# Optimization experiments

Measured on AMD Instinct MI355X. Metric: run time of the kernel, lower is better.

Reference implementation:

```python
import jax, jax.numpy as jnp
import numpy as np

# FUME epipolar image translation: for each output pixel p2=(x2,y2) the fundamental
# matrix F maps it to a line l = F @ [x2*d, y2*d, 1] in the input view (full-res
# coordinates; d = per-batch downsampling factor). The output value is the line
# integral of the input image along that epipolar line, computed by stepping one
# pixel at a time along the dominant axis with bilinear (1-D linear) interpolation
# across the other axis; out-of-bounds samples contribute zero.

def _translate(img, F, d):
    B, C, H, W = img.shape
    dt = img.dtype
    yy, xx = jnp.meshgrid(jnp.arange(H, dtype=dt), jnp.arange(W, dtype=dt), indexing='ij')
    db = d[:, None, None].astype(dt)                          # (B,1,1)
    px, py = xx[None] * db, yy[None] * db                     # (B,H,W) full-res coords
    a = F[0, 0] * px + F[0, 1] * py + F[0, 2]                 # line coeffs l = F @ [x,y,1]
    b = F[1, 0] * px + F[1, 1] * py + F[1, 2]
    c = F[2, 0] * px + F[2, 1] * py + F[2, 2]
    horiz = jnp.abs(b) >= jnp.abs(a)                          # dominant axis per pixel

    db4 = db[..., None]                                       # (B,1,1,1)
    # horizontal traversal: step over columns s, solve a*(s*d) + b*(y*d) + c = 0
    s = jnp.arange(W, dtype=dt)
    denom_h = jnp.where(horiz, b, jnp.ones((), dt))[..., None] * db4
    yline = -(a[..., None] * (s * db4) + c[..., None]) / denom_h    # (B,H,W,W)
    # vertical traversal: step over rows t, solve for x
    t = jnp.arange(H, dtype=dt)
    denom_v = jnp.where(horiz, jnp.ones((), dt), a)[..., None] * db4
    xline = -(b[..., None] * (t * db4) + c[..., None]) / denom_v    # (B,H,W,H)

    def sample_one(imgb, y, x):
        # imgb: (C,H,W); y: (H,W,W) row coord per column step; x: (H,W,H) col coord per row step
        y0 = jnp.floor(y)
        wy = y - y0
        y0i = jnp.clip(y0.astype(jnp.int32), 0, H - 1)
        y1i = jnp.clip(y0i + 1, 0, H - 1)
        cols = jnp.arange(W)
        vh = (1 - wy)[None] * imgb[:, y0i, cols] + wy[None] * imgb[:, y1i, cols]  # (C,H,W,W)
        vh = jnp.where(((y >= 0) & (y <= H - 1))[None], vh, jnp.zeros((), imgb.dtype)).sum(-1)

        x0 = jnp.floor(x)
        wx = x - x0
        x0i = jnp.clip(x0.astype(jnp.int32), 0, W - 1)
        x1i = jnp.clip(x0i + 1, 0, W - 1)
        rows = jnp.arange(H)
        vv = (1 - wx)[None] * imgb[:, rows, x0i] + wx[None] * imgb[:, rows, x1i]  # (C,H,W,H)
        vv = jnp.where(((x >= 0) & (x <= W - 1))[None], vv, jnp.zeros((), imgb.dtype)).sum(-1)
        return vh, vv

    vh, vv = jax.vmap(sample_one)(img, yline, xline)          # each (B,C,H,W)
    return jnp.where(horiz[:, None], vh, vv)


def setup_inputs() -> dict:
    key = jax.random.key(0)
    k1, k2, k3 = jax.random.split(key, 3)
    B, C, H, W = 4, 4, 128, 128
    view1 = jax.random.normal(k1, (B, C, H, W), jnp.float32)
    F21 = jax.random.normal(k2, (3, 3), jnp.float32)
    F12 = jax.random.normal(k3, (3, 3), jnp.float32)
    downsampled_factor = jnp.ones((B,), jnp.float32)
    return {"view1": view1, "F21": F21, "F12": F12, "downsampled_factor": downsampled_factor}


def reference(view1, F21, F12, downsampled_factor):
    # forward uses F21 only; F12 is kept for the backward pass in the original module
    return _translate(view1, F21, downsampled_factor)
```

## Files before the change

kernel.cpp:

```cpp
#include <hip/hip_runtime.h>


#define CC 4
#define HH 128
#define WW 128

__global__ void fume_stage(const float* __restrict__ img, float* __restrict__ ws) {
    __shared__ float tile[4][32][33];
    int tx0 = blockIdx.x * 32, ty0 = blockIdx.y * 32, b = blockIdx.z;
    int tx = threadIdx.x, ty = threadIdx.y;
    const float* src = img + (size_t)b * CC * HH * WW;
    #pragma unroll
    for (int ch = 0; ch < 4; ++ch)
        #pragma unroll
        for (int i = ty; i < 32; i += 8)
            tile[ch][i][tx] = src[(ch * HH + ty0 + i) * WW + tx0 + tx];
    __syncthreads();
    float4* base_h = (float4*)ws + (size_t)b * 32768;
    float4* base_v = base_h + 16384;
    #pragma unroll
    for (int i = ty; i < 32; i += 8) {
        float4 v = make_float4(tile[0][i][tx], tile[1][i][tx],
                               tile[2][i][tx], tile[3][i][tx]);
        base_v[(ty0 + i) * WW + (tx0 + tx)] = v;
        float4 h = make_float4(tile[0][tx][i], tile[1][tx][i],
                               tile[2][tx][i], tile[3][tx][i]);
        base_h[(tx0 + i) * HH + (ty0 + tx)] = h;
    }
}

__global__ void __launch_bounds__(512) fume_kernel(
        const float4* __restrict__ cubes,
        const float* __restrict__ F,
        const float* __restrict__ dsf,
        float* __restrict__ out) {
    int tx  = threadIdx.x;
    int seg = threadIdx.y;
    int x = blockIdx.x * 64 + tx;
    int y = blockIdx.y;
    int b = blockIdx.z;

    float d = dsf[b];
    float F00 = F[0], F01 = F[1], F02 = F[2];
    float F10 = F[3], F11 = F[4], F12 = F[5];
    float F20 = F[6], F21 = F[7], F22 = F[8];

    float px = __fmul_rn((float)x, d);
    float py = __fmul_rn((float)y, d);
    float av = __fadd_rn(__fadd_rn(__fmul_rn(F00, px), __fmul_rn(F01, py)), F02);
    float bv = __fadd_rn(__fadd_rn(__fmul_rn(F10, px), __fmul_rn(F11, py)), F12);
    float cv = __fadd_rn(__fadd_rn(__fmul_rn(F20, px), __fmul_rn(F21, py)), F22);

    bool horiz  = fabsf(bv) >= fabsf(av);
    float ncoef = horiz ? av : bv;
    float den   = __fmul_rn(horiz ? bv : av, d);
    float nrec  = -__fdiv_rn(1.0f, den);

    const float4* P = cubes + (size_t)b * 32768 + (horiz ? 0 : 16384);

    float A  = __fmul_rn(__fmul_rn(ncoef, d), nrec);
    float Bc = __fmul_rn(cv, nrec);
    int lkmin, lkmax;
    if (fabsf(A) > 1e-20f) {
        float inv = 1.0f / A;
        float k1 = (0.0f   - Bc) * inv;
        float k2 = (127.0f - Bc) * inv;
        float lo = fminf(k1, k2) - 2.0f;
        float hi = fmaxf(k1, k2) + 2.0f;
        lo = fmaxf(lo, 0.0f);
        hi = fminf(hi, 127.0f);
        if (lo > hi || !(lo == lo)) { lkmin = 1; lkmax = 0; }
        else { lkmin = (int)lo; lkmax = (int)hi; }
    } else {
        bool full = (Bc >= 0.0f) && (Bc <= 127.0f);
        lkmin = full ? 0 : 1;
        lkmax = full ? 127 : 0;
    }
    int wkmin = lkmin, wkmax = lkmax;
    #pragma unroll
    for (int off = 1; off < 64; off <<= 1) {
        wkmin = min(wkmin, __shfl_xor(wkmin, off));
        wkmax = max(wkmax, __shfl_xor(wkmax, off));
    }

    float a0 = 0.f, a1 = 0.f, a2 = 0.f, a3 = 0.f;
    int len = wkmax - wkmin + 1;
    if (len > 0) {
        int cnt = (len + 7) >> 3;
        int ks  = wkmin + seg * cnt;
        int ke  = min(ks + cnt - 1, wkmax);
        #pragma unroll 4
        for (int k = ks; k <= ke; ++k) {
            float m  = __fmul_rn((float)k, d);
            float q  = __fadd_rn(__fmul_rn(ncoef, m), cv);
            float u  = __fmul_rn(q, nrec);
            bool ok  = (u >= 0.f) && (u <= 127.f);
            int i0   = (int)floorf(u);
            i0 = max(0, min(i0, 126));
            float w  = __fsub_rn(u, (float)i0);
            float wz  = ok ? w : 0.f;
            float omw = ok ? __fsub_rn(1.f, w) : 0.f;
            const float4* row = P + k * 128;
            float4 q0 = row[i0];
            float4 q1 = row[i0 + 1];
            a0 = fmaf(omw, q0.x, a0); a0 = fmaf(wz, q1.x, a0);
            a1 = fmaf(omw, q0.y, a1); a1 = fmaf(wz, q1.y, a1);
            a2 = fmaf(omw, q0.z, a2); a2 = fmaf(wz, q1.z, a2);
            a3 = fmaf(omw, q0.w, a3); a3 = fmaf(wz, q1.w, a3);
        }
    }

    __shared__ float part[8][4][64];
    part[seg][0][tx] = a0;
    part[seg][1][tx] = a1;
    part[seg][2][tx] = a2;
    part[seg][3][tx] = a3;
    __syncthreads();

    if (seg < 4) {
        int ch = seg;
        float s = part[0][ch][tx];
        #pragma unroll
        for (int t = 1; t < 8; ++t) s = __fadd_rn(s, part[t][ch][tx]);
        out[(((size_t)b * CC + ch) * HH + y) * WW + x] = s;
    }
}

extern "C" void kernel_launch(void* const* d_in, const int* in_sizes, int n_in,
                              void* d_out, int out_size, void* d_ws, size_t ws_size,
                              hipStream_t stream) {
    const float* view1 = (const float*)d_in[0];
    const float* F21   = (const float*)d_in[1];
    const float* dsf   = (const float*)d_in[3];

    const int B = in_sizes[3];

    dim3 stb(32, 8, 1);
    dim3 stg(WW / 32, HH / 32, B);
    fume_stage<<<stg, stb, 0, stream>>>(view1, (float*)d_ws);

    dim3 ftb(64, 8, 1);
    dim3 ftg(WW / 64, HH, B);
    fume_kernel<<<ftg, ftb, 0, stream>>>((const float4*)d_ws, F21, dsf,
                                         (float*)d_out);
}
```

Before: 70.41 us.

## Pack neighbor pairs as fp16 and use fdot2 for interpolation

The staging kernel now stores each texel together with its right (or lower) neighbor as packed fp16 pairs for four channels in one 16-byte entry. The main loop then issues one gather per step instead of two and does the 2-tap interpolation with fdot2 instructions. This halves gather traffic and instruction count in the hot loop. The cost is fp16 precision on both image values and weights, which may exceed the reference tolerance. The staging tile also grows by one row and column to hold the halo.

```diff
diff --git a/kernel.cpp b/kernel.cpp
--- a/kernel.cpp
+++ b/kernel.cpp
@@ -5,27 +5,50 @@
 #define HH 128
 #define WW 128
 
-__global__ void fume_stage(const float* __restrict__ img, float* __restrict__ ws) {
-    __shared__ float tile[4][32][33];
+typedef _Float16 h2 __attribute__((ext_vector_type(2)));
+
+__global__ void fume_stage(const float* __restrict__ img, float4* __restrict__ ws) {
+    __shared__ float tile[4][33][33];
     int tx0 = blockIdx.x * 32, ty0 = blockIdx.y * 32, b = blockIdx.z;
     int tx = threadIdx.x, ty = threadIdx.y;
     const float* src = img + (size_t)b * CC * HH * WW;
+    int c32 = min(tx0 + 32, WW - 1);
     #pragma unroll
-    for (int ch = 0; ch < 4; ++ch)
-        #pragma unroll
-        for (int i = ty; i < 32; i += 8)
-            tile[ch][i][tx] = src[(ch * HH + ty0 + i) * WW + tx0 + tx];
+    for (int ch = 0; ch < 4; ++ch) {
+        for (int i = ty; i < 33; i += 8) {
+            int r = min(ty0 + i, HH - 1);
+            tile[ch][i][tx] = src[(ch * HH + r) * WW + tx0 + tx];
+            if (tx == 0) tile[ch][i][32] = src[(ch * HH + r) * WW + c32];
+        }
+    }
     __syncthreads();
-    float4* base_h = (float4*)ws + (size_t)b * 32768;
+
+    float4* base_h = ws + (size_t)b * 32768;
     float4* base_v = base_h + 16384;
     #pragma unroll
     for (int i = ty; i < 32; i += 8) {
-        float4 v = make_float4(tile[0][i][tx], tile[1][i][tx],
-                               tile[2][i][tx], tile[3][i][tx]);
-        base_v[(ty0 + i) * WW + (tx0 + tx)] = v;
-        float4 h = make_float4(tile[0][tx][i], tile[1][tx][i],
-                               tile[2][tx][i], tile[3][tx][i]);
-        base_h[(tx0 + i) * HH + (ty0 + tx)] = h;
+        {
+            h2 p0 = { (_Float16)tile[0][i][tx], (_Float16)tile[0][i][tx + 1] };
+            h2 p1 = { (_Float16)tile[1][i][tx], (_Float16)tile[1][i][tx + 1] };
+            h2 p2 = { (_Float16)tile[2][i][tx], (_Float16)tile[2][i][tx + 1] };
+            h2 p3 = { (_Float16)tile[3][i][tx], (_Float16)tile[3][i][tx + 1] };
+            float4 e = make_float4(__builtin_bit_cast(float, p0),
+                                   __builtin_bit_cast(float, p1),
+                                   __builtin_bit_cast(float, p2),
+                                   __builtin_bit_cast(float, p3));
+            base_v[(ty0 + i) * WW + (tx0 + tx)] = e;
+        }
+        {
+            h2 p0 = { (_Float16)tile[0][tx][i], (_Float16)tile[0][tx + 1][i] };
+            h2 p1 = { (_Float16)tile[1][tx][i], (_Float16)tile[1][tx + 1][i] };
+            h2 p2 = { (_Float16)tile[2][tx][i], (_Float16)tile[2][tx + 1][i] };
+            h2 p3 = { (_Float16)tile[3][tx][i], (_Float16)tile[3][tx + 1][i] };
+            float4 e = make_float4(__builtin_bit_cast(float, p0),
+                                   __builtin_bit_cast(float, p1),
+                                   __builtin_bit_cast(float, p2),
+                                   __builtin_bit_cast(float, p3));
+            base_h[(tx0 + i) * HH + (ty0 + tx)] = e;
+        }
     }
 }
 
@@ -65,10 +88,8 @@
         float inv = 1.0f / A;
         float k1 = (0.0f   - Bc) * inv;
         float k2 = (127.0f - Bc) * inv;
-        float lo = fminf(k1, k2) - 2.0f;
-        float hi = fmaxf(k1, k2) + 2.0f;
-        lo = fmaxf(lo, 0.0f);
-        hi = fminf(hi, 127.0f);
+        float lo = fmaxf(fminf(k1, k2) - 2.0f, 0.0f);
+        float hi = fminf(fmaxf(k1, k2) + 2.0f, 127.0f);
         if (lo > hi || !(lo == lo)) { lkmin = 1; lkmax = 0; }
         else { lkmin = (int)lo; lkmax = (int)hi; }
     } else {
@@ -100,13 +121,12 @@
             float w  = __fsub_rn(u, (float)i0);
             float wz  = ok ? w : 0.f;
             float omw = ok ? __fsub_rn(1.f, w) : 0.f;
-            const float4* row = P + k * 128;
-            float4 q0 = row[i0];
-            float4 q1 = row[i0 + 1];
-            a0 = fmaf(omw, q0.x, a0); a0 = fmaf(wz, q1.x, a0);
-            a1 = fmaf(omw, q0.y, a1); a1 = fmaf(wz, q1.y, a1);
-            a2 = fmaf(omw, q0.z, a2); a2 = fmaf(wz, q1.z, a2);
-            a3 = fmaf(omw, q0.w, a3); a3 = fmaf(wz, q1.w, a3);
+            h2 wp = { (_Float16)omw, (_Float16)wz };
+            float4 e = P[k * 128 + i0];
+            a0 = __builtin_amdgcn_fdot2(wp, __builtin_bit_cast(h2, e.x), a0, false);
+            a1 = __builtin_amdgcn_fdot2(wp, __builtin_bit_cast(h2, e.y), a1, false);
+            a2 = __builtin_amdgcn_fdot2(wp, __builtin_bit_cast(h2, e.z), a2, false);
+            a3 = __builtin_amdgcn_fdot2(wp, __builtin_bit_cast(h2, e.w), a3, false);
         }
     }
 
@@ -137,7 +157,7 @@
 
     dim3 stb(32, 8, 1);
     dim3 stg(WW / 32, HH / 32, B);
-    fume_stage<<<stg, stb, 0, stream>>>(view1, (float*)d_ws);
+    fume_stage<<<stg, stb, 0, stream>>>(view1, (float4*)d_ws);
 
     dim3 ftb(64, 8, 1);
     dim3 ftg(WW / 64, HH, B);
```

After: 78.85 us. +12.0%, slower.
